# Optimization experiments

Measured on AMD Instinct MI355X. Metric: run time of the kernel, lower is better.

Reference implementation:

```python
import jax, jax.numpy as jnp
import numpy as np

B, L, H, V = 2, 1024, 64, 32000
HID = 4 * H  # hidden_dim = num_harmonics * 4


def setup_inputs() -> dict:
    key = jax.random.key(0)
    ks = jax.random.split(key, 12)
    freqs = jax.random.normal(ks[0], (B, L, H), dtype=jnp.float32)
    amps = jax.random.uniform(ks[1], (B, L, H), dtype=jnp.float32)  # positive so log1p(sum) is finite
    phases = jax.random.normal(ks[2], (B, L, H), dtype=jnp.float32)
    wave_repr = jnp.concatenate([freqs, amps, phases], axis=-1)  # [B, L, 3H]
    s = 0.05
    return {
        "wave_repr": wave_repr,
        "vocab_frequencies": jax.random.normal(ks[3], (V, H), dtype=jnp.float32),
        "vocab_phases": jax.random.normal(ks[4], (V, H), dtype=jnp.float32) * 0.5,
        "W0": jax.random.normal(ks[5], (3 * H, HID), dtype=jnp.float32) * s,
        "b0": jnp.zeros((HID,), dtype=jnp.float32),
        "W1": jax.random.normal(ks[6], (HID, HID), dtype=jnp.float32) * s,
        "b1": jnp.zeros((HID,), dtype=jnp.float32),
        "W2": jax.random.normal(ks[7], (HID, HID), dtype=jnp.float32) * s,
        "b2": jnp.zeros((HID,), dtype=jnp.float32),
        "Wv": jax.random.normal(ks[8], (HID, V), dtype=jnp.float32) * s,
        "bv": jnp.zeros((V,), dtype=jnp.float32),
        "residual_weights": jnp.full((3,), 0.5, dtype=jnp.float32),
    }


def _gelu(x):
    return jax.nn.gelu(x, approximate=False)  # torch F.gelu default = exact erf


def reference(wave_repr, vocab_frequencies, vocab_phases, W0, b0, W1, b1, W2, b2, Wv, bv, residual_weights):
    h = vocab_frequencies.shape[1]
    freqs = wave_repr[..., :h]
    amps = wave_repr[..., h:2 * h]
    phases = wave_repr[..., 2 * h:]

    # synthesis MLP: layer 0 has no residual; layers 1..2 add weighted residual
    x = _gelu(wave_repr @ W0 + b0)
    for i, (W, b) in enumerate(((W1, b1), (W2, b2)), start=1):
        res = x
        x = _gelu(x @ W + b) + residual_weights[i] * res

    # freq_similarity = -cdist(freqs, vocab_frequencies): expanded as one GEMM
    f2 = jnp.sum(freqs * freqs, axis=-1, keepdims=True)           # [B,L,1]
    v2 = jnp.sum(vocab_frequencies * vocab_frequencies, axis=-1)  # [V]
    cross = jnp.einsum('blh,vh->blv', freqs, vocab_frequencies)   # [B,L,V]
    freq_similarity = -jnp.sqrt(jnp.maximum(f2 + v2 - 2.0 * cross, 0.0))

    # mean_h cos(phase - vocab_phase) via cos(a-b) = cos a cos b + sin a sin b (two GEMMs)
    phase_coherence = (
        jnp.einsum('blh,vh->blv', jnp.cos(phases), jnp.cos(vocab_phases))
        + jnp.einsum('blh,vh->blv', jnp.sin(phases), jnp.sin(vocab_phases))
    ) / h

    amp_energy = jnp.sum(amps, axis=-1, keepdims=True)  # [B,L,1]
    pattern_match = (freq_similarity + 0.5 * phase_coherence) * jnp.log1p(amp_energy)

    synthesis_proj = x @ Wv + bv  # [B,L,V]
    return pattern_match + 0.1 * synthesis_proj
```

## Files before the change

kernel.cpp:

```cpp
#include <hip/hip_runtime.h>
#include <hip/hip_bf16.h>

typedef unsigned short u16;
typedef __attribute__((ext_vector_type(8))) unsigned short u16x8;
typedef __attribute__((ext_vector_type(8))) short short8;
typedef __attribute__((ext_vector_type(4))) float f32x4;

#define VCOLS 32000
#define ASTRIDE 448
#define BSTRIDE 448

__device__ __forceinline__ u16 f2bf(float f) {
    union { float f; unsigned u; } x; x.f = f;
    unsigned r = x.u + 0x7FFF + ((x.u >> 16) & 1);
    return (u16)(r >> 16);
}

__device__ __forceinline__ float gelu_exact(float v) {
    return 0.5f * v * (1.0f + erff(v * 0.70710678118654752f));
}

__device__ __forceinline__ void gload_lds16(const void* g, void* l) {
    __builtin_amdgcn_global_load_lds(
        (const __attribute__((address_space(1))) unsigned int*)g,
        (__attribute__((address_space(3))) unsigned int*)l, 16, 0, 0);
}

#define RP_ROWS 8
__global__ __launch_bounds__(256) void row_prep(
    const float* __restrict__ wr,
    const float* __restrict__ W0, const float* __restrict__ b0,
    const float* __restrict__ W1, const float* __restrict__ b1,
    const float* __restrict__ W2, const float* __restrict__ b2,
    const float* __restrict__ rw,
    u16* __restrict__ Ag, float* __restrict__ rowstats)
{
    __shared__ float in_s[RP_ROWS * 192];
    __shared__ float x_s[RP_ROWS * 256];
    __shared__ float y_s[RP_ROWS * 256];
    __shared__ u16  row_s[RP_ROWS][448];
    __shared__ float la_s[RP_ROWS];

    const int t = threadIdx.x;
    const int r0 = blockIdx.x * RP_ROWS;

    for (int i = t; i < RP_ROWS * 192; i += 256)
        in_s[i] = wr[(size_t)r0 * 192 + i];
    __syncthreads();

    {
        int row = t >> 5, j = t & 31;
        float a0 = in_s[row*192 + j],      a1 = in_s[row*192 + 32 + j];
        float f2p = a0*a0 + a1*a1;
        float ampp = in_s[row*192 + 64 + j] + in_s[row*192 + 96 + j];
        #pragma unroll
        for (int m = 16; m >= 1; m >>= 1) {
            f2p  += __shfl_xor(f2p, m);
            ampp += __shfl_xor(ampp, m);
        }
        if (j == 0) {
            float la = log1pf(ampp);
            la_s[row] = la;
            rowstats[(size_t)(r0+row)*2]     = f2p;
            rowstats[(size_t)(r0+row)*2 + 1] = la;
        }
    }
    const float rw1 = rw[1], rw2 = rw[2];

    float acc[RP_ROWS], res[RP_ROWS];

    #pragma unroll
    for (int r = 0; r < RP_ROWS; ++r) acc[r] = 0.f;
    for (int k0 = 0; k0 < 192; k0 += 16) {
        float w[16];
        #pragma unroll
        for (int e = 0; e < 16; ++e) w[e] = W0[(k0+e)*256 + t];
        #pragma unroll
        for (int e = 0; e < 16; ++e) {
            #pragma unroll
            for (int r = 0; r < RP_ROWS; ++r) acc[r] += in_s[r*192 + k0 + e] * w[e];
        }
    }
    {
        float bb = b0[t];
        #pragma unroll
        for (int r = 0; r < RP_ROWS; ++r) {
            float v = gelu_exact(acc[r] + bb);
            res[r] = v; x_s[r*256 + t] = v;
        }
    }
    __syncthreads();

    #pragma unroll
    for (int r = 0; r < RP_ROWS; ++r) acc[r] = 0.f;
    for (int k0 = 0; k0 < 256; k0 += 16) {
        float w[16];
        #pragma unroll
        for (int e = 0; e < 16; ++e) w[e] = W1[(k0+e)*256 + t];
        #pragma unroll
        for (int e = 0; e < 16; ++e) {
            #pragma unroll
            for (int r = 0; r < RP_ROWS; ++r) acc[r] += x_s[r*256 + k0 + e] * w[e];
        }
    }
    {
        float bb = b1[t];
        #pragma unroll
        for (int r = 0; r < RP_ROWS; ++r) {
            float v = gelu_exact(acc[r] + bb) + rw1 * res[r];
            res[r] = v; y_s[r*256 + t] = v;
        }
    }
    __syncthreads();

    #pragma unroll
    for (int r = 0; r < RP_ROWS; ++r) acc[r] = 0.f;
    for (int k0 = 0; k0 < 256; k0 += 16) {
        float w[16];
        #pragma unroll
        for (int e = 0; e < 16; ++e) w[e] = W2[(k0+e)*256 + t];
        #pragma unroll
        for (int e = 0; e < 16; ++e) {
            #pragma unroll
            for (int r = 0; r < RP_ROWS; ++r) acc[r] += y_s[r*256 + k0 + e] * w[e];
        }
    }
    {
        float bb = b2[t];
        #pragma unroll
        for (int r = 0; r < RP_ROWS; ++r)
            res[r] = gelu_exact(acc[r] + bb) + rw2 * res[r];
    }

    #pragma unroll
    for (int r = 0; r < RP_ROWS; ++r)
        row_s[r][192 + t] = f2bf(0.1f * res[r]);
    if (t < 64) {
        #pragma unroll
        for (int r = 0; r < RP_ROWS; ++r)
            row_s[r][t] = f2bf(in_s[r*192 + t]);
    } else if (t < 128) {
        int h = t - 64;
        #pragma unroll
        for (int r = 0; r < RP_ROWS; ++r) {
            float s, c; __sincosf(in_s[r*192 + 128 + h], &s, &c);
            row_s[r][t] = f2bf(c * (0.5f/64.f) * la_s[r]);
        }
    } else if (t < 192) {
        int h = t - 128;
        #pragma unroll
        for (int r = 0; r < RP_ROWS; ++r) {
            float s, c; __sincosf(in_s[r*192 + 128 + h], &s, &c);
            row_s[r][t] = f2bf(s * (0.5f/64.f) * la_s[r]);
        }
    }
    __syncthreads();

    for (int idx = t; idx < RP_ROWS * 56; idx += 256) {
        int r = idx / 56, c = idx % 56;
        int kt = c >> 3, ac = c & 7;
        int m = r0 + r;
        u16x8 val = *(const u16x8*)&row_s[r][c*8];
        *(u16x8*)(Ag + (size_t)m*ASTRIDE + kt*64 + ((ac ^ (m & 7)) * 8)) = val;
    }
}

__global__ __launch_bounds__(256) void vocab_prep(
    const float* __restrict__ vf, const float* __restrict__ vp,
    const float* __restrict__ Wv,
    u16* __restrict__ Bg, float* __restrict__ v2)
{
    __shared__ float wv_s[64][68];

    const int t = threadIdx.x;
    const int v0 = blockIdx.x * 64;

    {
        int v = v0 + (t >> 2);
        int q = t & 3;
        int s = v & 7;
        u16x8* baseB = (u16x8*)(Bg + (size_t)v * BSTRIDE);

        const float4* src = (const float4*)(vf + (size_t)v*64 + q*16);
        float ss = 0.f;
        u16 tf[16];
        #pragma unroll
        for (int i = 0; i < 4; ++i) {
            float4 x = src[i];
            ss += x.x*x.x + x.y*x.y + x.z*x.z + x.w*x.w;
            tf[i*4+0] = f2bf(x.x); tf[i*4+1] = f2bf(x.y);
            tf[i*4+2] = f2bf(x.z); tf[i*4+3] = f2bf(x.w);
        }
        u16x8 o0, o1;
        #pragma unroll
        for (int e = 0; e < 8; ++e) { o0[e] = tf[e]; o1[e] = tf[8+e]; }
        baseB[(2*q) ^ s]     = o0;
        baseB[(2*q+1) ^ s]   = o1;

        ss += __shfl_xor(ss, 1);
        ss += __shfl_xor(ss, 2);
        if (q == 0) v2[v] = ss;

        const float4* sp = (const float4*)(vp + (size_t)v*64 + q*16);
        u16 tc[16], ts_[16];
        #pragma unroll
        for (int i = 0; i < 4; ++i) {
            float4 x = sp[i];
            float sn, cs;
            __sincosf(x.x, &sn, &cs); tc[i*4+0] = f2bf(cs); ts_[i*4+0] = f2bf(sn);
            __sincosf(x.y, &sn, &cs); tc[i*4+1] = f2bf(cs); ts_[i*4+1] = f2bf(sn);
            __sincosf(x.z, &sn, &cs); tc[i*4+2] = f2bf(cs); ts_[i*4+2] = f2bf(sn);
            __sincosf(x.w, &sn, &cs); tc[i*4+3] = f2bf(cs); ts_[i*4+3] = f2bf(sn);
        }
        u16x8 c0, c1, s0, s1;
        #pragma unroll
        for (int e = 0; e < 8; ++e) { c0[e]=tc[e]; c1[e]=tc[8+e]; s0[e]=ts_[e]; s1[e]=ts_[8+e]; }
        baseB[8  + ((2*q) ^ s)]   = c0;
        baseB[8  + ((2*q+1) ^ s)] = c1;
        baseB[16 + ((2*q) ^ s)]   = s0;
        baseB[16 + ((2*q+1) ^ s)] = s1;
    }

    for (int kc = 0; kc < 4; ++kc) {
        __syncthreads();
        {
            int r = t >> 2, q = t & 3;
            const float4* src = (const float4*)(Wv + (size_t)(kc*64 + r)*VCOLS + v0 + q*16);
            float4* dst = (float4*)&wv_s[r][q*16];
            dst[0] = src[0]; dst[1] = src[1]; dst[2] = src[2]; dst[3] = src[3];
        }
        __syncthreads();
        {
            int v = t & 63, g = t >> 6;
            int s = (v0 + v) & 7;
            u16x8* baseB = (u16x8*)(Bg + (size_t)(v0 + v) * BSTRIDE);
            #pragma unroll
            for (int cc = 0; cc < 2; ++cc) {
                int ch = g*2 + cc;
                u16x8 o;
                #pragma unroll
                for (int e = 0; e < 8; ++e) o[e] = f2bf(wv_s[ch*8 + e][v]);
                baseB[(3 + kc)*8 + (ch ^ s)] = o;
            }
        }
    }
}

__global__ __launch_bounds__(256, 3) void spectral_main(
    const u16* __restrict__ Ag, const u16* __restrict__ Bg,
    const float* __restrict__ rowstats, const float* __restrict__ v2,
    const float* __restrict__ bv, float* __restrict__ out)
{
    __shared__ u16 As[128 * 64];
    __shared__ u16 Bs[128 * 64];

    const int bid = blockIdx.x;
    const int l   = (bid & 7) * 500 + (bid >> 3);
    const int tm  = l / 250;
    const int tn  = l % 250;
    const int rowA0 = tm * 128;
    const int colB0 = tn * 128;

    const int tid  = threadIdx.x;
    const int wv   = tid >> 6, lane = tid & 63;
    const int wm   = (wv >> 1) * 64, wn = (wv & 1) * 64;
    const int cg   = lane >> 4, ln = lane & 15;

    f32x4 acc[4][4] = {};

    auto stage = [&](int kt) {
        const u16* ab = Ag + (size_t)(rowA0 + wv*32 + (lane >> 3)) * ASTRIDE + kt*64 + (lane & 7)*8;
        u16* al = As + wv*2048 + lane*8;
        #pragma unroll
        for (int c = 0; c < 4; ++c)
            gload_lds16(ab + (size_t)c*8*ASTRIDE, al + c*512);
        const u16* bb = Bg + (size_t)(colB0 + wv*32 + (lane >> 3)) * BSTRIDE + kt*64 + (lane & 7)*8;
        u16* bl = Bs + wv*2048 + lane*8;
        #pragma unroll
        for (int c = 0; c < 4; ++c)
            gload_lds16(bb + (size_t)c*8*BSTRIDE, bl + c*512);
    };

    auto compute = [&]() {
        #pragma unroll
        for (int kk = 0; kk < 2; ++kk) {
            short8 a[4], b[4];
            #pragma unroll
            for (int fr = 0; fr < 4; ++fr) {
                int r = wm + fr*16 + ln;
                a[fr] = *(const short8*)&As[r*64 + (((kk*4 + cg) ^ (ln & 7)) * 8)];
            }
            #pragma unroll
            for (int fc = 0; fc < 4; ++fc) {
                int r = wn + fc*16 + ln;
                b[fc] = *(const short8*)&Bs[r*64 + (((kk*4 + cg) ^ (ln & 7)) * 8)];
            }
            #pragma unroll
            for (int fr = 0; fr < 4; ++fr)
                #pragma unroll
                for (int fc = 0; fc < 4; ++fc)
                    acc[fr][fc] = __builtin_amdgcn_mfma_f32_16x16x32_bf16(
                        a[fr], b[fc], acc[fr][fc], 0, 0, 0);
        }
    };

    stage(0);
    for (int kt = 0; kt < 7; ++kt) {
        __syncthreads();
        compute();

        if (kt == 0) {
            float f2m[4][4], lam[4][4], v2n[4], bvn[4];
            #pragma unroll
            for (int fr = 0; fr < 4; ++fr)
                #pragma unroll
                for (int j = 0; j < 4; ++j) {
                    int m = rowA0 + wm + fr*16 + cg*4 + j;
                    f2m[fr][j] = rowstats[(size_t)2*m];
                    lam[fr][j] = rowstats[(size_t)2*m + 1];
                }
            #pragma unroll
            for (int fc = 0; fc < 4; ++fc) {
                int n = colB0 + wn + fc*16 + ln;
                v2n[fc] = v2[n];
                bvn[fc] = bv[n];
            }
            #pragma unroll
            for (int fr = 0; fr < 4; ++fr)
                #pragma unroll
                for (int fc = 0; fc < 4; ++fc)
                    #pragma unroll
                    for (int j = 0; j < 4; ++j) {
                        float cross = acc[fr][fc][j];
                        float arg = fmaxf(f2m[fr][j] + v2n[fc] - 2.0f*cross, 0.0f);
                        acc[fr][fc][j] = 0.1f*bvn[fc] - lam[fr][j]*sqrtf(arg);
                    }
        }

        __syncthreads();
        if (kt < 6) stage(kt + 1);
    }

    #pragma unroll
    for (int fr = 0; fr < 4; ++fr)
        #pragma unroll
        for (int fc = 0; fc < 4; ++fc)
            #pragma unroll
            for (int j = 0; j < 4; ++j) {
                int m = rowA0 + wm + fr*16 + cg*4 + j;
                int n = colB0 + wn + fc*16 + ln;
                out[(size_t)m * VCOLS + n] = acc[fr][fc][j];
            }
}

extern "C" void kernel_launch(void* const* d_in, const int* in_sizes, int n_in,
                              void* d_out, int out_size, void* d_ws, size_t ws_size,
                              hipStream_t stream) {
    const float* wave_repr = (const float*)d_in[0];
    const float* vf  = (const float*)d_in[1];
    const float* vp  = (const float*)d_in[2];
    const float* W0  = (const float*)d_in[3];
    const float* b0  = (const float*)d_in[4];
    const float* W1  = (const float*)d_in[5];
    const float* b1  = (const float*)d_in[6];
    const float* W2  = (const float*)d_in[7];
    const float* b2  = (const float*)d_in[8];
    const float* Wv  = (const float*)d_in[9];
    const float* bv  = (const float*)d_in[10];
    const float* rw  = (const float*)d_in[11];
    float* out = (float*)d_out;

    u16*   Ag       = (u16*)d_ws;
    u16*   Bg       = (u16*)((char*)d_ws + 1835008);
    float* rowstats = (float*)((char*)d_ws + 30507008);
    float* v2       = (float*)((char*)d_ws + 30523392);

    hipLaunchKernelGGL(row_prep, dim3(2048 / RP_ROWS), dim3(256), 0, stream,
                       wave_repr, W0, b0, W1, b1, W2, b2, rw, Ag, rowstats);
    hipLaunchKernelGGL(vocab_prep, dim3(VCOLS / 64), dim3(256), 0, stream,
                       vf, vp, Wv, Bg, v2);
    hipLaunchKernelGGL(spectral_main, dim3(16 * 250), dim3(256), 0, stream,
                       Ag, Bg, rowstats, v2, bv, out);
}
```

Before: 446.4 us.

## Merge row and vocab prep kernels into one launch with halved row blocks

Result: faster. 432.2 us (-3.2%).

```diff
diff --git a/kernel.cpp b/kernel.cpp
--- a/kernel.cpp
+++ b/kernel.cpp
@@ -26,8 +26,22 @@
         (__attribute__((address_space(3))) unsigned int*)l, 16, 0, 0);
 }
 
-#define RP_ROWS 8
-__global__ __launch_bounds__(256) void row_prep(
+#define RP_ROWS 4
+#define NVBLK 500
+
+struct RowSh {
+    float in_s[RP_ROWS * 192];
+    float x_s[RP_ROWS * 256];
+    float y_s[RP_ROWS * 256];
+    u16   row_s[RP_ROWS][448];
+    float la_s[RP_ROWS];
+};
+struct VocSh {
+    float wv[64][68];
+};
+union PrepSh { RowSh r; VocSh v; };
+
+__device__ void row_mode(PrepSh* sh, int rblk,
     const float* __restrict__ wr,
     const float* __restrict__ W0, const float* __restrict__ b0,
     const float* __restrict__ W1, const float* __restrict__ b1,
@@ -35,32 +49,27 @@
     const float* __restrict__ rw,
     u16* __restrict__ Ag, float* __restrict__ rowstats)
 {
-    __shared__ float in_s[RP_ROWS * 192];
-    __shared__ float x_s[RP_ROWS * 256];
-    __shared__ float y_s[RP_ROWS * 256];
-    __shared__ u16  row_s[RP_ROWS][448];
-    __shared__ float la_s[RP_ROWS];
-
+    RowSh& S = sh->r;
     const int t = threadIdx.x;
-    const int r0 = blockIdx.x * RP_ROWS;
+    const int r0 = rblk * RP_ROWS;
 
     for (int i = t; i < RP_ROWS * 192; i += 256)
-        in_s[i] = wr[(size_t)r0 * 192 + i];
+        S.in_s[i] = wr[(size_t)r0 * 192 + i];
     __syncthreads();
 
     {
-        int row = t >> 5, j = t & 31;
-        float a0 = in_s[row*192 + j],      a1 = in_s[row*192 + 32 + j];
-        float f2p = a0*a0 + a1*a1;
-        float ampp = in_s[row*192 + 64 + j] + in_s[row*192 + 96 + j];
-        #pragma unroll
-        for (int m = 16; m >= 1; m >>= 1) {
+        int row = t >> 6, j = t & 63;
+        float f = S.in_s[row*192 + j];
+        float f2p  = f * f;
+        float ampp = S.in_s[row*192 + 64 + j];
+        #pragma unroll
+        for (int m = 32; m >= 1; m >>= 1) {
             f2p  += __shfl_xor(f2p, m);
             ampp += __shfl_xor(ampp, m);
         }
         if (j == 0) {
             float la = log1pf(ampp);
-            la_s[row] = la;
+            S.la_s[row] = la;
             rowstats[(size_t)(r0+row)*2]     = f2p;
             rowstats[(size_t)(r0+row)*2 + 1] = la;
         }
@@ -78,7 +87,7 @@
         #pragma unroll
         for (int e = 0; e < 16; ++e) {
             #pragma unroll
-            for (int r = 0; r < RP_ROWS; ++r) acc[r] += in_s[r*192 + k0 + e] * w[e];
+            for (int r = 0; r < RP_ROWS; ++r) acc[r] += S.in_s[r*192 + k0 + e] * w[e];
         }
     }
     {
@@ -86,7 +95,7 @@
         #pragma unroll
         for (int r = 0; r < RP_ROWS; ++r) {
             float v = gelu_exact(acc[r] + bb);
-            res[r] = v; x_s[r*256 + t] = v;
+            res[r] = v; S.x_s[r*256 + t] = v;
         }
     }
     __syncthreads();
@@ -100,7 +109,7 @@
         #pragma unroll
         for (int e = 0; e < 16; ++e) {
             #pragma unroll
-            for (int r = 0; r < RP_ROWS; ++r) acc[r] += x_s[r*256 + k0 + e] * w[e];
+            for (int r = 0; r < RP_ROWS; ++r) acc[r] += S.x_s[r*256 + k0 + e] * w[e];
         }
     }
     {
@@ -108,7 +117,7 @@
         #pragma unroll
         for (int r = 0; r < RP_ROWS; ++r) {
             float v = gelu_exact(acc[r] + bb) + rw1 * res[r];
-            res[r] = v; y_s[r*256 + t] = v;
+            res[r] = v; S.y_s[r*256 + t] = v;
         }
     }
     __syncthreads();
@@ -122,7 +131,7 @@
         #pragma unroll
         for (int e = 0; e < 16; ++e) {
             #pragma unroll
-            for (int r = 0; r < RP_ROWS; ++r) acc[r] += y_s[r*256 + k0 + e] * w[e];
+            for (int r = 0; r < RP_ROWS; ++r) acc[r] += S.y_s[r*256 + k0 + e] * w[e];
         }
     }
     {
@@ -134,46 +143,48 @@
 
     #pragma unroll
     for (int r = 0; r < RP_ROWS; ++r)
-        row_s[r][192 + t] = f2bf(0.1f * res[r]);
+        S.row_s[r][192 + t] = f2bf(0.1f * res[r]);
     if (t < 64) {
         #pragma unroll
         for (int r = 0; r < RP_ROWS; ++r)
-            row_s[r][t] = f2bf(in_s[r*192 + t]);
+            S.row_s[r][t] = f2bf(S.in_s[r*192 + t]);
     } else if (t < 128) {
         int h = t - 64;
         #pragma unroll
         for (int r = 0; r < RP_ROWS; ++r) {
-            float s, c; __sincosf(in_s[r*192 + 128 + h], &s, &c);
-            row_s[r][t] = f2bf(c * (0.5f/64.f) * la_s[r]);
+            float s, c; __sincosf(S.in_s[r*192 + 128 + h], &s, &c);
+            S.row_s[r][t] = f2bf(c * (0.5f/64.f) * S.la_s[r]);
         }
     } else if (t < 192) {
         int h = t - 128;
         #pragma unroll
         for (int r = 0; r < RP_ROWS; ++r) {
-            float s, c; __sincosf(in_s[r*192 + 128 + h], &s, &c);
-            row_s[r][t] = f2bf(s * (0.5f/64.f) * la_s[r]);
+            float s, c; __sincosf(S.in_s[r*192 + 128 + h], &s, &c);
+            S.row_s[r][t] = f2bf(s * (0.5f/64.f) * S.la_s[r]);
         }
     }
     __syncthreads();
 
-    for (int idx = t; idx < RP_ROWS * 56; idx += 256) {
-        int r = idx / 56, c = idx % 56;
-        int kt = c >> 3, ac = c & 7;
-        int m = r0 + r;
-        u16x8 val = *(const u16x8*)&row_s[r][c*8];
-        *(u16x8*)(Ag + (size_t)m*ASTRIDE + kt*64 + ((ac ^ (m & 7)) * 8)) = val;
-    }
-}
-
-__global__ __launch_bounds__(256) void vocab_prep(
+    {
+        int idx = t;
+        if (idx < RP_ROWS * 56) {
+            int r = idx / 56, c = idx % 56;
+            int kt = c >> 3, ac = c & 7;
+            int m = r0 + r;
+            u16x8 val = *(const u16x8*)&S.row_s[r][c*8];
+            *(u16x8*)(Ag + (size_t)m*ASTRIDE + kt*64 + ((ac ^ (m & 7)) * 8)) = val;
+        }
+    }
+}
+
+__device__ void vocab_mode(PrepSh* sh, int vblk,
     const float* __restrict__ vf, const float* __restrict__ vp,
     const float* __restrict__ Wv,
     u16* __restrict__ Bg, float* __restrict__ v2)
 {
-    __shared__ float wv_s[64][68];
-
+    VocSh& S = sh->v;
     const int t = threadIdx.x;
-    const int v0 = blockIdx.x * 64;
+    const int v0 = vblk * 64;
 
     {
         int v = v0 + (t >> 2);
@@ -226,7 +237,7 @@
         {
             int r = t >> 2, q = t & 3;
             const float4* src = (const float4*)(Wv + (size_t)(kc*64 + r)*VCOLS + v0 + q*16);
-            float4* dst = (float4*)&wv_s[r][q*16];
+            float4* dst = (float4*)&S.wv[r][q*16];
             dst[0] = src[0]; dst[1] = src[1]; dst[2] = src[2]; dst[3] = src[3];
         }
         __syncthreads();
@@ -239,11 +250,30 @@
                 int ch = g*2 + cc;
                 u16x8 o;
                 #pragma unroll
-                for (int e = 0; e < 8; ++e) o[e] = f2bf(wv_s[ch*8 + e][v]);
+                for (int e = 0; e < 8; ++e) o[e] = f2bf(S.wv[ch*8 + e][v]);
                 baseB[(3 + kc)*8 + (ch ^ s)] = o;
             }
         }
     }
+}
+
+__global__ __launch_bounds__(256) void prep_all(
+    const float* __restrict__ wr,
+    const float* __restrict__ W0, const float* __restrict__ b0,
+    const float* __restrict__ W1, const float* __restrict__ b1,
+    const float* __restrict__ W2, const float* __restrict__ b2,
+    const float* __restrict__ rw,
+    const float* __restrict__ vf, const float* __restrict__ vp,
+    const float* __restrict__ Wv,
+    u16* __restrict__ Ag, u16* __restrict__ Bg,
+    float* __restrict__ rowstats, float* __restrict__ v2)
+{
+    __shared__ PrepSh sh;
+    const int bid = blockIdx.x;
+    if (bid < NVBLK)
+        vocab_mode(&sh, bid, vf, vp, Wv, Bg, v2);
+    else
+        row_mode(&sh, bid - NVBLK, wr, W0, b0, W1, b1, W2, b2, rw, Ag, rowstats);
 }
 
 __global__ __launch_bounds__(256, 3) void spectral_main(
@@ -375,10 +405,9 @@
     float* rowstats = (float*)((char*)d_ws + 30507008);
     float* v2       = (float*)((char*)d_ws + 30523392);
 
-    hipLaunchKernelGGL(row_prep, dim3(2048 / RP_ROWS), dim3(256), 0, stream,
-                       wave_repr, W0, b0, W1, b1, W2, b2, rw, Ag, rowstats);
-    hipLaunchKernelGGL(vocab_prep, dim3(VCOLS / 64), dim3(256), 0, stream,
-                       vf, vp, Wv, Bg, v2);
+    hipLaunchKernelGGL(prep_all, dim3(NVBLK + 2048 / RP_ROWS), dim3(256), 0, stream,
+                       wave_repr, W0, b0, W1, b1, W2, b2, rw,
+                       vf, vp, Wv, Ag, Bg, rowstats, v2);
     hipLaunchKernelGGL(spectral_main, dim3(16 * 250), dim3(256), 0, stream,
                        Ag, Bg, rowstats, v2, bv, out);
 }
```
